# Performance work log

Measured on AMD Instinct MI355X. Metric: run time of the kernel, lower is better.

The kernel has to match this reference:

```python
import jax, jax.numpy as jnp
import numpy as np

K = 3        # kernel_size
DIL = 1      # dilation
PAD = 1      # padding (replicate)
RANKS = 3
STAGES = 9
C_OUT = 32


def setup_inputs() -> dict:
    key = jax.random.key(0)
    k1, k2, k3 = jax.random.split(key, 3)
    b, cin, H, W = 2, 3, 160, 160
    x = jax.random.normal(k1, (b, cin, H, W), dtype=jnp.float32)
    head_w = jax.random.normal(k2, (C_OUT, cin), dtype=jnp.float32) * (1.0 / np.sqrt(cin))
    tail_w = jax.random.normal(k3, (cin, C_OUT), dtype=jnp.float32) * (1.0 / np.sqrt(C_OUT))
    alphas = jnp.full((STAGES,), 0.01, dtype=jnp.float32)
    betas = jnp.full((STAGES,), 0.01, dtype=jnp.float32)
    return {"x": x, "head_w": head_w, "tail_w": tail_w, "alphas": alphas, "betas": betas}


def _unfold_like_torch(xp, H, W):
    # xp: [b, C, H+2p, W+2p] replicate-padded. Reproduce torch nn.Unfold output
    # layout [b, C*k*k, H*W] (channel-major, then ki, kj; L row-major over h,w).
    b, C = xp.shape[0], xp.shape[1]
    cols = [xp[:, :, i * DIL:i * DIL + H, j * DIL:j * DIL + W]
            for i in range(K) for j in range(K)]
    patches = jnp.stack(cols, axis=2)            # [b, C, k*k, H, W]
    return patches.reshape(b, C * K * K, H * W)  # torch unfold layout


def reference(x, head_w, tail_w, alphas, betas):
    b, cin, H, W = x.shape
    # head 1x1 conv (no bias) + relu
    xh = jax.nn.relu(jnp.einsum('bchw,oc->bohw', x, head_w))
    xp = jnp.pad(xh, ((0, 0), (0, 0), (PAD, PAD), (PAD, PAD)), mode='edge')
    Xu = _unfold_like_torch(xp, H, W)                 # [b, C*kk, H*W]
    # Faithful to torch: X = unfold.view(b, C, H, W, -1) (row-major reinterpret)
    X = Xu.reshape(b, C_OUT, H, W, K * K)
    U = jnp.repeat(X.mean(axis=-1, keepdims=True), RANKS, axis=-1)  # [b,C,H,W,r]
    V = jnp.repeat(X.mean(axis=1, keepdims=True), RANKS, axis=1)    # [b,r,H,W,kk]
    for i in range(STAGES):
        num_V = jnp.einsum('bchwr,bchwk->brhwk', U, X)
        UV = jnp.einsum('bchwr,brhwk->bchwk', U, V)
        den_V = jnp.einsum('bchwr,bchwk->brhwk', U, UV)
        V = V - betas[i] * (den_V - num_V)
        num_U = jnp.einsum('bchwk,brhwk->bchwr', X, V)
        UV = jnp.einsum('bchwr,brhwk->bchwk', U, V)
        den_U = jnp.einsum('bchwk,brhwk->bchwr', UV, V)
        U = U - alphas[i] * (den_U - num_U)
    center = (K // 2) * K + K // 2
    UVc = jnp.einsum('bchwr,brhwk->bchwk', U, V)[..., center]  # [b,C,H,W]
    out = jax.nn.relu(jnp.einsum('bchw,oc->bohw', UVc, tail_w))
    return out
```

## Files before the change

### kernel.cpp

```cpp
#include <hip/hip_runtime.h>
#include <hip/hip_bf16.h>

#define NB    2
#define HW    25600
#define WDIM  160
#define NSTG  9

template <int CTRL>
__device__ __forceinline__ float dpp_add(float v) {
    int moved = __builtin_amdgcn_update_dpp(0, __float_as_int(v), CTRL, 0xf, 0xf, true);
    return v + __int_as_float(moved);
}

__device__ __forceinline__ float reduce4(float v) {
    v = dpp_add<0xB1>(v);
    v = dpp_add<0x4E>(v);
    return v;
}

__global__ __launch_bounds__(256, 3) void fused_kernel(const float* __restrict__ x,
                                                       const float* __restrict__ head_w,
                                                       const float* __restrict__ tail_w,
                                                       const float* __restrict__ alphas,
                                                       const float* __restrict__ betas,
                                                       float* __restrict__ out) {
    int sub = threadIdx.x & 3;
    int pid = blockIdx.x * 64 + (threadIdx.x >> 2);
    int b   = blockIdx.x / 400;
    int s2  = pid - b * HW;

    int c0 = sub * 8;
    float hw[8][3];
#pragma unroll
    for (int j = 0; j < 8; ++j)
#pragma unroll
        for (int ci = 0; ci < 3; ++ci)
            hw[j][ci] = head_w[(c0 + j) * 3 + ci];

    const float* xb0 = x + b * 3 * HW;
    const float* xb1 = xb0 + HW;
    const float* xb2 = xb1 + HW;

    int g9  = s2 * 9;
    int kk0 = g9 / HW;
    int r0  = g9 - kk0 * HW;
    int h0  = r0 / WDIM;
    int w0  = r0 - h0 * WDIM;
    int ki0 = kk0 / 3;
    int dh0 = ki0 - 1,            dw0 = kk0 - ki0 * 3 - 1;
    int kk1 = kk0 + 1;
    int ki1 = kk1 / 3;
    int dh1 = ki1 - 1,            dw1 = kk1 - ki1 * 3 - 1;

    float X[9][8];
#pragma unroll
    for (int k2 = 0; k2 < 9; ++k2) {
        int r  = r0 + k2;
        int wn = w0 + k2;
        int cw = (wn >= WDIM);
        int w1 = cw ? wn - WDIM : wn;
        int h1 = h0 + cw;
        bool wr = (r >= HW);
        int h  = wr ? 0 : h1;
        int w  = wr ? r - HW : w1;
        int dh = wr ? dh1 : dh0;
        int dw = wr ? dw1 : dw0;
        int hh = min(max(h + dh, 0), 159);
        int ww = min(max(w + dw, 0), 159);
        int p  = hh * WDIM + ww;
        float x0 = xb0[p], x1 = xb1[p], x2 = xb2[p];
#pragma unroll
        for (int j = 0; j < 8; ++j)
            X[k2][j] = fmaxf(hw[j][0] * x0 + hw[j][1] * x1 + hw[j][2] * x2, 0.f);
    }

    float u[8];
#pragma unroll
    for (int j = 0; j < 8; ++j) {
        float a = X[0][j];
#pragma unroll
        for (int k = 1; k < 9; ++k) a += X[k][j];
        u[j] = a * (1.f / 9.f);
    }
    float v[9];
#pragma unroll
    for (int k = 0; k < 9; ++k) {
        float pr = ((X[k][0] + X[k][1]) + (X[k][2] + X[k][3]))
                 + ((X[k][4] + X[k][5]) + (X[k][6] + X[k][7]));
        v[k] = reduce4(pr) * (1.f / 32.f);
    }

#pragma unroll
    for (int i = 0; i < NSTG; ++i) {
        float b3 = 3.f * betas[i];
        float a3 = 3.f * alphas[i];
        float beta  = betas[i];
        float alpha = alphas[i];
        float sp = ((u[0] * u[0] + u[1] * u[1]) + (u[2] * u[2] + u[3] * u[3]))
                 + ((u[4] * u[4] + u[5] * u[5]) + (u[6] * u[6] + u[7] * u[7]));
        float s  = reduce4(sp);
        float vs = 1.f - b3 * s;
#pragma unroll
        for (int k = 0; k < 9; ++k) {
            float qp = u[0] * X[k][0];
#pragma unroll
            for (int j = 1; j < 8; ++j) qp += u[j] * X[k][j];
            float q = reduce4(qp);
            v[k] = v[k] * vs + beta * q;
        }
        float t = (((v[0] * v[0] + v[1] * v[1]) + (v[2] * v[2] + v[3] * v[3]))
                +  ((v[4] * v[4] + v[5] * v[5]) + (v[6] * v[6] + v[7] * v[7])))
                +  v[8] * v[8];
        float us = 1.f - a3 * t;
#pragma unroll
        for (int j = 0; j < 8; ++j) {
            float m = X[0][j] * v[0];
#pragma unroll
            for (int k = 1; k < 9; ++k) m += X[k][j] * v[k];
            u[j] = u[j] * us + alpha * m;
        }
    }

    float v4 = v[4];
    float uvc[8];
#pragma unroll
    for (int j = 0; j < 8; ++j) uvc[j] = 3.f * u[j] * v4;
    float o[3];
#pragma unroll
    for (int oo = 0; oo < 3; ++oo) {
        const float* tw = tail_w + oo * 32 + c0;
        float pr = ((uvc[0] * tw[0] + uvc[1] * tw[1]) + (uvc[2] * tw[2] + uvc[3] * tw[3]))
                 + ((uvc[4] * tw[4] + uvc[5] * tw[5]) + (uvc[6] * tw[6] + uvc[7] * tw[7]));
        o[oo] = fmaxf(reduce4(pr), 0.f);
    }
    if (sub == 0) {
        float* op = out + b * 3 * HW + s2;
        op[0]      = o[0];
        op[HW]     = o[1];
        op[2 * HW] = o[2];
    }
}

extern "C" void kernel_launch(void* const* d_in, const int* in_sizes, int n_in,
                              void* d_out, int out_size, void* d_ws, size_t ws_size,
                              hipStream_t stream) {
    const float* x      = (const float*)d_in[0];
    const float* head_w = (const float*)d_in[1];
    const float* tail_w = (const float*)d_in[2];
    const float* alphas = (const float*)d_in[3];
    const float* betas  = (const float*)d_in[4];
    float*       out    = (float*)d_out;

    fused_kernel<<<dim3(NB * HW * 4 / 256), dim3(256), 0, stream>>>(
        x, head_w, tail_w, alphas, betas, out);
}
```

Measured before the change: 75.84 us.

## Split channels over 8 lanes and process two pixels per thread

Result: slower. 82.80 us (+9.2%).

```diff
diff --git a/kernel.cpp b/kernel.cpp
--- a/kernel.cpp
+++ b/kernel.cpp
@@ -12,9 +12,10 @@
     return v + __int_as_float(moved);
 }
 
-__device__ __forceinline__ float reduce4(float v) {
+__device__ __forceinline__ float reduce8(float v) {
     v = dpp_add<0xB1>(v);
     v = dpp_add<0x4E>(v);
+    v = dpp_add<0x141>(v);
     return v;
 }
 
@@ -24,120 +25,137 @@
                                                        const float* __restrict__ alphas,
                                                        const float* __restrict__ betas,
                                                        float* __restrict__ out) {
-    int sub = threadIdx.x & 3;
-    int pid = blockIdx.x * 64 + (threadIdx.x >> 2);
+    int sub = threadIdx.x & 7;
+    int g   = (threadIdx.x >> 3) & 7;
+    int wib = threadIdx.x >> 6;
     int b   = blockIdx.x / 400;
-    int s2  = pid - b * HW;
+    int base = blockIdx.x * 64 + wib * 16 - b * HW;
+    int s2[2] = { base + g, base + 8 + g };
 
-    int c0 = sub * 8;
-    float hw[8][3];
+    int c0 = sub * 4;
+    float hwv[4][3];
 #pragma unroll
-    for (int j = 0; j < 8; ++j)
+    for (int j = 0; j < 4; ++j)
 #pragma unroll
         for (int ci = 0; ci < 3; ++ci)
-            hw[j][ci] = head_w[(c0 + j) * 3 + ci];
+            hwv[j][ci] = head_w[(c0 + j) * 3 + ci];
 
     const float* xb0 = x + b * 3 * HW;
     const float* xb1 = xb0 + HW;
     const float* xb2 = xb1 + HW;
 
-    int g9  = s2 * 9;
-    int kk0 = g9 / HW;
-    int r0  = g9 - kk0 * HW;
-    int h0  = r0 / WDIM;
-    int w0  = r0 - h0 * WDIM;
-    int ki0 = kk0 / 3;
-    int dh0 = ki0 - 1,            dw0 = kk0 - ki0 * 3 - 1;
-    int kk1 = kk0 + 1;
-    int ki1 = kk1 / 3;
-    int dh1 = ki1 - 1,            dw1 = kk1 - ki1 * 3 - 1;
-
-    float X[9][8];
+    float X[2][9][4];
 #pragma unroll
-    for (int k2 = 0; k2 < 9; ++k2) {
-        int r  = r0 + k2;
-        int wn = w0 + k2;
-        int cw = (wn >= WDIM);
-        int w1 = cw ? wn - WDIM : wn;
-        int h1 = h0 + cw;
-        bool wr = (r >= HW);
-        int h  = wr ? 0 : h1;
-        int w  = wr ? r - HW : w1;
-        int dh = wr ? dh1 : dh0;
-        int dw = wr ? dw1 : dw0;
-        int hh = min(max(h + dh, 0), 159);
-        int ww = min(max(w + dw, 0), 159);
-        int p  = hh * WDIM + ww;
-        float x0 = xb0[p], x1 = xb1[p], x2 = xb2[p];
+    for (int px = 0; px < 2; ++px) {
+        int ss  = s2[px];
+        int g9  = ss * 9;
+        int kk0 = g9 / HW;
+        int r0  = g9 - kk0 * HW;
+        int h0  = r0 / WDIM;
+        int w0  = r0 - h0 * WDIM;
+        int ki0 = kk0 / 3;
+        int dh0 = ki0 - 1, dw0 = kk0 - ki0 * 3 - 1;
+        int kk1 = kk0 + 1;
+        int ki1 = kk1 / 3;
+        int dh1 = ki1 - 1, dw1 = kk1 - ki1 * 3 - 1;
 #pragma unroll
-        for (int j = 0; j < 8; ++j)
-            X[k2][j] = fmaxf(hw[j][0] * x0 + hw[j][1] * x1 + hw[j][2] * x2, 0.f);
+        for (int k2 = 0; k2 < 9; ++k2) {
+            int r  = r0 + k2;
+            int wn = w0 + k2;
+            int cw = (wn >= WDIM);
+            int w1 = cw ? wn - WDIM : wn;
+            int h1 = h0 + cw;
+            bool wr = (r >= HW);
+            int h  = wr ? 0 : h1;
+            int w  = wr ? r - HW : w1;
+            int dh = wr ? dh1 : dh0;
+            int dw = wr ? dw1 : dw0;
+            int hh = min(max(h + dh, 0), 159);
+            int ww = min(max(w + dw, 0), 159);
+            int p  = hh * WDIM + ww;
+            float x0 = xb0[p], x1 = xb1[p], x2 = xb2[p];
+#pragma unroll
+            for (int j = 0; j < 4; ++j)
+                X[px][k2][j] = fmaxf(hwv[j][0] * x0 + hwv[j][1] * x1 + hwv[j][2] * x2, 0.f);
+        }
     }
 
-    float u[8];
+    float u[2][4];
 #pragma unroll
-    for (int j = 0; j < 8; ++j) {
-        float a = X[0][j];
+    for (int px = 0; px < 2; ++px)
 #pragma unroll
-        for (int k = 1; k < 9; ++k) a += X[k][j];
-        u[j] = a * (1.f / 9.f);
-    }
-    float v[9];
+        for (int j = 0; j < 4; ++j) {
+            float a = X[px][0][j];
 #pragma unroll
-    for (int k = 0; k < 9; ++k) {
-        float pr = ((X[k][0] + X[k][1]) + (X[k][2] + X[k][3]))
-                 + ((X[k][4] + X[k][5]) + (X[k][6] + X[k][7]));
-        v[k] = reduce4(pr) * (1.f / 32.f);
+            for (int k = 1; k < 9; ++k) a += X[px][k][j];
+            u[px][j] = a * (1.f / 9.f);
+        }
+    float v[2][9];
+#pragma unroll
+    for (int k = 0; k < 9; ++k)
+#pragma unroll
+        for (int px = 0; px < 2; ++px) {
+            float pr = (X[px][k][0] + X[px][k][1]) + (X[px][k][2] + X[px][k][3]);
+            v[px][k] = reduce8(pr) * (1.f / 32.f);
+        }
+
+#pragma unroll
+    for (int i = 0; i < NSTG; ++i) {
+        float beta  = betas[i];
+        float alpha = alphas[i];
+        float vs[2];
+#pragma unroll
+        for (int px = 0; px < 2; ++px) {
+            float sp = (u[px][0] * u[px][0] + u[px][1] * u[px][1])
+                     + (u[px][2] * u[px][2] + u[px][3] * u[px][3]);
+            vs[px] = 1.f - 3.f * beta * reduce8(sp);
+        }
+#pragma unroll
+        for (int k = 0; k < 9; ++k)
+#pragma unroll
+            for (int px = 0; px < 2; ++px) {
+                float qp = (u[px][0] * X[px][k][0] + u[px][1] * X[px][k][1])
+                         + (u[px][2] * X[px][k][2] + u[px][3] * X[px][k][3]);
+                float q  = reduce8(qp);
+                v[px][k] = v[px][k] * vs[px] + beta * q;
+            }
+#pragma unroll
+        for (int px = 0; px < 2; ++px) {
+            float t = ((v[px][0] * v[px][0] + v[px][1] * v[px][1])
+                     + (v[px][2] * v[px][2] + v[px][3] * v[px][3]))
+                    + ((v[px][4] * v[px][4] + v[px][5] * v[px][5])
+                     + (v[px][6] * v[px][6] + v[px][7] * v[px][7]))
+                    +  v[px][8] * v[px][8];
+            float us = 1.f - 3.f * alpha * t;
+#pragma unroll
+            for (int j = 0; j < 4; ++j) {
+                float m = X[px][0][j] * v[px][0];
+#pragma unroll
+                for (int k = 1; k < 9; ++k) m += X[px][k][j] * v[px][k];
+                u[px][j] = u[px][j] * us + alpha * m;
+            }
+        }
     }
 
 #pragma unroll
-    for (int i = 0; i < NSTG; ++i) {
-        float b3 = 3.f * betas[i];
-        float a3 = 3.f * alphas[i];
-        float beta  = betas[i];
-        float alpha = alphas[i];
-        float sp = ((u[0] * u[0] + u[1] * u[1]) + (u[2] * u[2] + u[3] * u[3]))
-                 + ((u[4] * u[4] + u[5] * u[5]) + (u[6] * u[6] + u[7] * u[7]));
-        float s  = reduce4(sp);
-        float vs = 1.f - b3 * s;
+    for (int px = 0; px < 2; ++px) {
+        float v4 = v[px][4];
+        float uvc[4];
 #pragma unroll
-        for (int k = 0; k < 9; ++k) {
-            float qp = u[0] * X[k][0];
+        for (int j = 0; j < 4; ++j) uvc[j] = 3.f * u[px][j] * v4;
+        float o[3];
 #pragma unroll
-            for (int j = 1; j < 8; ++j) qp += u[j] * X[k][j];
-            float q = reduce4(qp);
-            v[k] = v[k] * vs + beta * q;
+        for (int oo = 0; oo < 3; ++oo) {
+            const float* tw = tail_w + oo * 32 + c0;
+            float pr = (uvc[0] * tw[0] + uvc[1] * tw[1]) + (uvc[2] * tw[2] + uvc[3] * tw[3]);
+            o[oo] = fmaxf(reduce8(pr), 0.f);
         }
-        float t = (((v[0] * v[0] + v[1] * v[1]) + (v[2] * v[2] + v[3] * v[3]))
-                +  ((v[4] * v[4] + v[5] * v[5]) + (v[6] * v[6] + v[7] * v[7])))
-                +  v[8] * v[8];
-        float us = 1.f - a3 * t;
-#pragma unroll
-        for (int j = 0; j < 8; ++j) {
-            float m = X[0][j] * v[0];
-#pragma unroll
-            for (int k = 1; k < 9; ++k) m += X[k][j] * v[k];
-            u[j] = u[j] * us + alpha * m;
+        if (sub == 0) {
+            float* op = out + b * 3 * HW + s2[px];
+            op[0]      = o[0];
+            op[HW]     = o[1];
+            op[2 * HW] = o[2];
         }
-    }
-
-    float v4 = v[4];
-    float uvc[8];
-#pragma unroll
-    for (int j = 0; j < 8; ++j) uvc[j] = 3.f * u[j] * v4;
-    float o[3];
-#pragma unroll
-    for (int oo = 0; oo < 3; ++oo) {
-        const float* tw = tail_w + oo * 32 + c0;
-        float pr = ((uvc[0] * tw[0] + uvc[1] * tw[1]) + (uvc[2] * tw[2] + uvc[3] * tw[3]))
-                 + ((uvc[4] * tw[4] + uvc[5] * tw[5]) + (uvc[6] * tw[6] + uvc[7] * tw[7]));
-        o[oo] = fmaxf(reduce4(pr), 0.f);
-    }
-    if (sub == 0) {
-        float* op = out + b * 3 * HW + s2;
-        op[0]      = o[0];
-        op[HW]     = o[1];
-        op[2 * HW] = o[2];
     }
 }
 
@@ -151,6 +169,6 @@
     const float* betas  = (const float*)d_in[4];
     float*       out    = (float*)d_out;
 
-    fused_kernel<<<dim3(NB * HW * 4 / 256), dim3(256), 0, stream>>>(
+    fused_kernel<<<dim3(NB * HW / 64), dim3(256), 0, stream>>>(
         x, head_w, tail_w, alphas, betas, out);
 }
```

## Split each pixel's 32 channels across 16 lanes instead of 4

Applied to the files above, without the earlier changes.

New measurement: 85.88 us. 1.13x slower.

```diff
diff --git a/kernel.cpp b/kernel.cpp
--- a/kernel.cpp
+++ b/kernel.cpp
@@ -12,30 +12,29 @@
     return v + __int_as_float(moved);
 }
 
-__device__ __forceinline__ float reduce4(float v) {
+__device__ __forceinline__ float reduce16(float v) {
     v = dpp_add<0xB1>(v);
     v = dpp_add<0x4E>(v);
+    v = dpp_add<0x141>(v);
+    v = dpp_add<0x140>(v);
     return v;
 }
 
-__global__ __launch_bounds__(256, 3) void fused_kernel(const float* __restrict__ x,
+__global__ __launch_bounds__(256, 8) void fused_kernel(const float* __restrict__ x,
                                                        const float* __restrict__ head_w,
                                                        const float* __restrict__ tail_w,
                                                        const float* __restrict__ alphas,
                                                        const float* __restrict__ betas,
                                                        float* __restrict__ out) {
-    int sub = threadIdx.x & 3;
-    int pid = blockIdx.x * 64 + (threadIdx.x >> 2);
-    int b   = blockIdx.x / 400;
+    int sub = threadIdx.x & 15;
+    int pid = blockIdx.x * 16 + (threadIdx.x >> 4);
+    int b   = blockIdx.x / 1600;
     int s2  = pid - b * HW;
 
-    int c0 = sub * 8;
-    float hw[8][3];
-#pragma unroll
-    for (int j = 0; j < 8; ++j)
-#pragma unroll
-        for (int ci = 0; ci < 3; ++ci)
-            hw[j][ci] = head_w[(c0 + j) * 3 + ci];
+    int c0 = sub * 2;
+    const float* hwp = head_w + c0 * 3;
+    float hw00 = hwp[0], hw01 = hwp[1], hw02 = hwp[2];
+    float hw10 = hwp[3], hw11 = hwp[4], hw12 = hwp[5];
 
     const float* xb0 = x + b * 3 * HW;
     const float* xb1 = xb0 + HW;
@@ -47,12 +46,12 @@
     int h0  = r0 / WDIM;
     int w0  = r0 - h0 * WDIM;
     int ki0 = kk0 / 3;
-    int dh0 = ki0 - 1,            dw0 = kk0 - ki0 * 3 - 1;
+    int dh0 = ki0 - 1, dw0 = kk0 - ki0 * 3 - 1;
     int kk1 = kk0 + 1;
     int ki1 = kk1 / 3;
-    int dh1 = ki1 - 1,            dw1 = kk1 - ki1 * 3 - 1;
+    int dh1 = ki1 - 1, dw1 = kk1 - ki1 * 3 - 1;
 
-    float X[9][8];
+    float X[9][2];
 #pragma unroll
     for (int k2 = 0; k2 < 9; ++k2) {
         int r  = r0 + k2;
@@ -69,69 +68,54 @@
         int ww = min(max(w + dw, 0), 159);
         int p  = hh * WDIM + ww;
         float x0 = xb0[p], x1 = xb1[p], x2 = xb2[p];
-#pragma unroll
-        for (int j = 0; j < 8; ++j)
-            X[k2][j] = fmaxf(hw[j][0] * x0 + hw[j][1] * x1 + hw[j][2] * x2, 0.f);
+        X[k2][0] = fmaxf(hw00 * x0 + hw01 * x1 + hw02 * x2, 0.f);
+        X[k2][1] = fmaxf(hw10 * x0 + hw11 * x1 + hw12 * x2, 0.f);
     }
 
-    float u[8];
+    float u[2];
 #pragma unroll
-    for (int j = 0; j < 8; ++j) {
-        float a = X[0][j];
-#pragma unroll
-        for (int k = 1; k < 9; ++k) a += X[k][j];
+    for (int j = 0; j < 2; ++j) {
+        float a = (((X[0][j] + X[1][j]) + (X[2][j] + X[3][j]))
+                +  ((X[4][j] + X[5][j]) + (X[6][j] + X[7][j]))) + X[8][j];
         u[j] = a * (1.f / 9.f);
     }
     float v[9];
 #pragma unroll
-    for (int k = 0; k < 9; ++k) {
-        float pr = ((X[k][0] + X[k][1]) + (X[k][2] + X[k][3]))
-                 + ((X[k][4] + X[k][5]) + (X[k][6] + X[k][7]));
-        v[k] = reduce4(pr) * (1.f / 32.f);
-    }
+    for (int k = 0; k < 9; ++k)
+        v[k] = reduce16(X[k][0] + X[k][1]) * (1.f / 32.f);
 
 #pragma unroll
     for (int i = 0; i < NSTG; ++i) {
-        float b3 = 3.f * betas[i];
-        float a3 = 3.f * alphas[i];
         float beta  = betas[i];
         float alpha = alphas[i];
-        float sp = ((u[0] * u[0] + u[1] * u[1]) + (u[2] * u[2] + u[3] * u[3]))
-                 + ((u[4] * u[4] + u[5] * u[5]) + (u[6] * u[6] + u[7] * u[7]));
-        float s  = reduce4(sp);
-        float vs = 1.f - b3 * s;
+        float s  = reduce16(u[0] * u[0] + u[1] * u[1]);
+        float vs = 1.f - 3.f * beta * s;
 #pragma unroll
         for (int k = 0; k < 9; ++k) {
-            float qp = u[0] * X[k][0];
-#pragma unroll
-            for (int j = 1; j < 8; ++j) qp += u[j] * X[k][j];
-            float q = reduce4(qp);
+            float q = reduce16(u[0] * X[k][0] + u[1] * X[k][1]);
             v[k] = v[k] * vs + beta * q;
         }
         float t = (((v[0] * v[0] + v[1] * v[1]) + (v[2] * v[2] + v[3] * v[3]))
                 +  ((v[4] * v[4] + v[5] * v[5]) + (v[6] * v[6] + v[7] * v[7])))
-                +  v[8] * v[8];
-        float us = 1.f - a3 * t;
+                +   v[8] * v[8];
+        float us = 1.f - 3.f * alpha * t;
 #pragma unroll
-        for (int j = 0; j < 8; ++j) {
-            float m = X[0][j] * v[0];
-#pragma unroll
-            for (int k = 1; k < 9; ++k) m += X[k][j] * v[k];
+        for (int j = 0; j < 2; ++j) {
+            float m = ((X[0][j] * v[0] + X[1][j] * v[1]) + (X[2][j] * v[2] + X[3][j] * v[3]))
+                    + ((X[4][j] * v[4] + X[5][j] * v[5]) + (X[6][j] * v[6] + X[7][j] * v[7]))
+                    +   X[8][j] * v[8];
             u[j] = u[j] * us + alpha * m;
         }
     }
 
     float v4 = v[4];
-    float uvc[8];
-#pragma unroll
-    for (int j = 0; j < 8; ++j) uvc[j] = 3.f * u[j] * v4;
+    float uvc0 = 3.f * u[0] * v4;
+    float uvc1 = 3.f * u[1] * v4;
     float o[3];
 #pragma unroll
     for (int oo = 0; oo < 3; ++oo) {
         const float* tw = tail_w + oo * 32 + c0;
-        float pr = ((uvc[0] * tw[0] + uvc[1] * tw[1]) + (uvc[2] * tw[2] + uvc[3] * tw[3]))
-                 + ((uvc[4] * tw[4] + uvc[5] * tw[5]) + (uvc[6] * tw[6] + uvc[7] * tw[7]));
-        o[oo] = fmaxf(reduce4(pr), 0.f);
+        o[oo] = fmaxf(reduce16(uvc0 * tw[0] + uvc1 * tw[1]), 0.f);
     }
     if (sub == 0) {
         float* op = out + b * 3 * HW + s2;
@@ -151,6 +135,6 @@
     const float* betas  = (const float*)d_in[4];
     float*       out    = (float*)d_out;
 
-    fused_kernel<<<dim3(NB * HW * 4 / 256), dim3(256), 0, stream>>>(
+    fused_kernel<<<dim3(NB * HW / 16), dim3(256), 0, stream>>>(
         x, head_w, tail_w, alphas, betas, out);
 }
```
